# Performance work log

Hardware: AMD Instinct MI355X
Metric: run time of the kernel (lower is better)

Reference implementation:

```python
import jax, jax.numpy as jnp
import numpy as np

B, T, H = 8, 2048, 2048
N = 100000
PROJ = 512
TOP_K = 10
LN_EPS = 1e-5


def setup_inputs() -> dict:
    key = jax.random.key(0)
    ks = jax.random.split(key, 16)
    s = 0.02
    return {
        "x": jax.random.normal(ks[0], (B, T, H), jnp.float32),
        "keys": jax.random.normal(ks[1], (N, H), jnp.float32),
        "confidences": jax.random.uniform(ks[2], (N,), jnp.float32),
        "Wq": jax.random.normal(ks[3], (PROJ, H), jnp.float32) * s,
        "bq": jnp.zeros((PROJ,), jnp.float32),
        "Wk": jax.random.normal(ks[4], (PROJ, H), jnp.float32) * s,
        "bk": jnp.zeros((PROJ,), jnp.float32),
        "Wg": jax.random.normal(ks[5], (H, 2 * H), jnp.float32) * s,
        "bg": jnp.zeros((H,), jnp.float32),
        "Wm1": jax.random.normal(ks[6], (H, 2 * H), jnp.float32) * s,
        "bm1": jnp.zeros((H,), jnp.float32),
        "Wm2": jax.random.normal(ks[7], (H, H), jnp.float32) * s,
        "bm2": jnp.zeros((H,), jnp.float32),
        "gamma": jnp.ones((H,), jnp.float32),
        "beta": jnp.zeros((H,), jnp.float32),
    }


def reference(x, keys, confidences, Wq, bq, Wk, bk, Wg, bg, Wm1, bm1, Wm2, bm2, gamma, beta):
    # query = mean over time: (B, H)
    query = x.mean(axis=1)
    # projections
    q = query @ Wq.T + bq                  # (B, 512)
    k_proj = keys @ Wk.T + bk              # (N, 512)
    # confidence-scaled scores and top-k retrieval
    scores = (q @ k_proj.T) * confidences[None, :]   # (B, N)
    _, top_idx = jax.lax.top_k(scores, TOP_K)        # (B, k)
    retrieved = keys[top_idx]                        # (B, k, H) gather
    mem_summary = retrieved.mean(axis=1)             # (B, H)
    gate_input = jnp.concatenate([query, mem_summary], axis=-1)  # (B, 2H)
    gate = jax.nn.sigmoid(gate_input @ Wg.T + bg)[:, None, :]    # (B, 1, H)
    h = jax.nn.gelu(gate_input @ Wm1.T + bm1, approximate=False)
    mem_integrated = (h @ Wm2.T + bm2)[:, None, :]               # (B, 1, H)
    y = x + gate * mem_integrated
    # LayerNorm over last dim
    mu = y.mean(axis=-1, keepdims=True)
    var = jnp.mean(jnp.square(y - mu), axis=-1, keepdims=True)
    return (y - mu) * jax.lax.rsqrt(var + LN_EPS) * gamma + beta
```

## Files before the change

### kernel.cpp

```cpp
#include <hip/hip_runtime.h>
#include <math.h>

constexpr int B    = 8;
constexpr int T    = 2048;
constexpr int H    = 2048;
constexpr int NK   = 100000;
constexpr int PROJ = 512;
constexpr int TOPK = 10;
constexpr int TCHUNK = 64;
constexpr int TSUB   = T / TCHUNK;
constexpr int NCHUNK = 64;
constexpr int CS     = 1600;

#define NEG_INF -3.4e38f

typedef float vfloat4 __attribute__((ext_vector_type(4)));

__global__ void __launch_bounds__(256) k_partial_sum(const float* __restrict__ x,
                                                     float* __restrict__ partial) {
    int hblk = blockIdx.x & 1;
    int tc   = (blockIdx.x >> 1) & 63;
    int b    = blockIdx.x >> 7;
    int h    = hblk * 1024 + threadIdx.x * 4;
    const float* xp = x + ((size_t)b * T + (size_t)tc * TSUB) * H + h;
    float4 acc = make_float4(0.f, 0.f, 0.f, 0.f);
#pragma unroll 4
    for (int t = 0; t < TSUB; ++t) {
        float4 v = *(const float4*)(xp + (size_t)t * H);
        acc.x += v.x; acc.y += v.y; acc.z += v.z; acc.w += v.w;
    }
    *(float4*)(partial + ((size_t)(b * TCHUNK + tc)) * H + h) = acc;
}

__global__ void __launch_bounds__(256) k_finish_mean(const float* __restrict__ partial,
                                                     float* __restrict__ query,
                                                     float* __restrict__ gi) {
    int idx = blockIdx.x * 256 + threadIdx.x;
    int b = idx >> 11, h = idx & 2047;
    float s = 0.f;
    for (int tc = 0; tc < TCHUNK; ++tc)
        s += partial[((size_t)(b * TCHUNK + tc)) * H + h];
    float m = s * (1.0f / T);
    query[idx] = m;
    gi[(size_t)b * 2 * H + h] = m;
}

__global__ void __launch_bounds__(256) k_q(const float* __restrict__ query,
                                           const float* __restrict__ Wq,
                                           const float* __restrict__ bq,
                                           float* __restrict__ qv) {
    int wave = threadIdx.x >> 6, lane = threadIdx.x & 63;
    int gidx = blockIdx.x * 4 + wave;
    int b = gidx >> 9, p = gidx & 511;
    const float* qr = query + (size_t)b * H;
    const float* wr = Wq + (size_t)p * H;
    float acc = 0.f;
#pragma unroll
    for (int j = lane * 4; j < H; j += 256) {
        float4 a = *(const float4*)(qr + j);
        float4 w = *(const float4*)(wr + j);
        acc += a.x * w.x + a.y * w.y + a.z * w.z + a.w * w.w;
    }
    for (int o = 32; o > 0; o >>= 1) acc += __shfl_down(acc, o, 64);
    if (lane == 0) qv[gidx] = acc + bq[p];
}

__global__ void k_qb(const float* __restrict__ qv, const float* __restrict__ bk,
                     float* __restrict__ qb) {
    int lane = threadIdx.x;
    for (int b = 0; b < B; ++b) {
        float acc = 0.f;
        for (int j = lane; j < PROJ; j += 64) acc += qv[b * PROJ + j] * bk[j];
        for (int o = 32; o > 0; o >>= 1) acc += __shfl_down(acc, o, 64);
        if (lane == 0) qb[b] = acc;
    }
}

__global__ void __launch_bounds__(256) k_qk_partial(const float* __restrict__ qv,
                                                    const float* __restrict__ Wk,
                                                    float* __restrict__ pqk) {
    int hblk = blockIdx.x & 7, pc = blockIdx.x >> 3;
    int h = hblk * 256 + threadIdx.x;
    float acc[B];
#pragma unroll
    for (int b = 0; b < B; ++b) acc[b] = 0.f;
    for (int p = pc * 32; p < pc * 32 + 32; ++p) {
        float w = Wk[(size_t)p * H + h];
#pragma unroll
        for (int b = 0; b < B; ++b) acc[b] += qv[b * PROJ + p] * w;
    }
#pragma unroll
    for (int b = 0; b < B; ++b)
        pqk[((size_t)(pc * B + b)) * H + h] = acc[b];
}

__global__ void __launch_bounds__(256) k_qk_finish(const float* __restrict__ pqk,
                                                   float* __restrict__ qk) {
    int idx = blockIdx.x * 256 + threadIdx.x;
    int b = idx >> 11, h = idx & 2047;
    float s = 0.f;
#pragma unroll
    for (int pc = 0; pc < 16; ++pc) s += pqk[((size_t)(pc * B + b)) * H + h];
    qk[idx] = s;
}

__global__ void __launch_bounds__(512) k_scores(const float* __restrict__ keys,
                                                const float* __restrict__ conf,
                                                const float* __restrict__ qk,
                                                const float* __restrict__ qb,
                                                float* __restrict__ scores) {
    __shared__ float sqk[B * H];
    for (int i = threadIdx.x * 4; i < B * H; i += 2048)
        *(float4*)(sqk + i) = *(const float4*)(qk + i);
    __syncthreads();

    const int wave = threadIdx.x >> 6, lane = threadIdx.x & 63;
    const long r0 = (long)blockIdx.x * 32 + wave * 4;

    float acc[4][B];
#pragma unroll
    for (int r = 0; r < 4; ++r)
#pragma unroll
        for (int b = 0; b < B; ++b) acc[r][b] = 0.f;

#pragma unroll 2
    for (int it = 0; it < 8; ++it) {
        int j = it * 256 + lane * 4;
        vfloat4 kv[4];
#pragma unroll
        for (int r = 0; r < 4; ++r)
            kv[r] = __builtin_nontemporal_load(
                (const vfloat4*)(keys + (size_t)(r0 + r) * H + j));
#pragma unroll
        for (int b = 0; b < B; ++b) {
            float4 w = *(const float4*)(sqk + b * H + j);
#pragma unroll
            for (int r = 0; r < 4; ++r)
                acc[r][b] += kv[r].x * w.x + kv[r].y * w.y + kv[r].z * w.z + kv[r].w * w.w;
        }
    }

#pragma unroll
    for (int r = 0; r < 4; ++r) {
        long n = r0 + r;
#pragma unroll
        for (int b = 0; b < B; ++b) {
            float v = acc[r][b];
            for (int o = 32; o > 0; o >>= 1) v += __shfl_down(v, o, 64);
            if (lane == 0)
                scores[(size_t)b * NK + n] = conf[n] * (v + qb[b]);
        }
    }
}

__global__ void __launch_bounds__(256) k_topk1(const float* __restrict__ scores,
                                               float* __restrict__ candv,
                                               int* __restrict__ candi) {
    const int c = blockIdx.x & (NCHUNK - 1), b = blockIdx.x >> 6;
    const int tid = threadIdx.x, lane = tid & 63, wave = tid >> 6;
    __shared__ float wv[4 * TOPK];
    __shared__ int   wi[4 * TOPK];

    float lv[TOPK];
    int   li[TOPK];
#pragma unroll
    for (int i = 0; i < TOPK; ++i) { lv[i] = NEG_INF; li[i] = 0; }

    const int start = c * CS;
    const int end = (start + CS < NK) ? start + CS : NK;
    for (int n = start + tid; n < end; n += 256) {
        float v = scores[(size_t)b * NK + n];
        if (v > lv[TOPK - 1]) {
            bool m[TOPK];
#pragma unroll
            for (int i = 0; i < TOPK; ++i) m[i] = (lv[i] < v);
#pragma unroll
            for (int i = TOPK - 1; i > 0; --i)
                if (m[i - 1]) { lv[i] = lv[i - 1]; li[i] = li[i - 1]; }
#pragma unroll
            for (int i = 0; i < TOPK; ++i)
                if (m[i] && (i == 0 || !m[i - 1])) { lv[i] = v; li[i] = n; }
        }
    }

    int ptr = 0;
    for (int round = 0; round < TOPK; ++round) {
        float bv = (ptr < TOPK) ? lv[ptr] : NEG_INF;
        int   bi = (ptr < TOPK) ? li[ptr] : 0;
        int   bl = lane;
        for (int o = 32; o > 0; o >>= 1) {
            float ov = __shfl_down(bv, o, 64);
            int   oi = __shfl_down(bi, o, 64);
            int   ol = __shfl_down(bl, o, 64);
            if (ov > bv) { bv = ov; bi = oi; bl = ol; }
        }
        if (lane == 0) { wv[wave * TOPK + round] = bv; wi[wave * TOPK + round] = bi; }
        bl = __shfl(bl, 0, 64);
        if (lane == bl) ptr++;
    }
    __syncthreads();

    if (wave == 0) {
        float v = (lane < 4 * TOPK) ? wv[lane] : NEG_INF;
        int  id = (lane < 4 * TOPK) ? wi[lane] : 0;
        for (int round = 0; round < TOPK; ++round) {
            float bv = v; int bi = id; int bl = lane;
            for (int o = 32; o > 0; o >>= 1) {
                float ov = __shfl_down(bv, o, 64);
                int   oi = __shfl_down(bi, o, 64);
                int   ol = __shfl_down(bl, o, 64);
                if (ov > bv) { bv = ov; bi = oi; bl = ol; }
            }
            if (lane == 0) {
                candv[(size_t)(b * NCHUNK + c) * TOPK + round] = bv;
                candi[(size_t)(b * NCHUNK + c) * TOPK + round] = bi;
            }
            bl = __shfl(bl, 0, 64);
            if (lane == bl) v = NEG_INF;
        }
    }
}

__global__ void __launch_bounds__(64) k_topk2(const float* __restrict__ candv,
                                              const int* __restrict__ candi,
                                              int* __restrict__ topidx) {
    const int b = blockIdx.x, lane = threadIdx.x;
    float lv[TOPK];
    int   li[TOPK];
#pragma unroll
    for (int i = 0; i < TOPK; ++i) { lv[i] = NEG_INF; li[i] = 0; }

#pragma unroll
    for (int r = 0; r < TOPK; ++r) {
        float v = candv[(size_t)b * NCHUNK * TOPK + lane * TOPK + r];
        int  id = candi[(size_t)b * NCHUNK * TOPK + lane * TOPK + r];
        if (v > lv[TOPK - 1]) {
            bool m[TOPK];
#pragma unroll
            for (int i = 0; i < TOPK; ++i) m[i] = (lv[i] < v);
#pragma unroll
            for (int i = TOPK - 1; i > 0; --i)
                if (m[i - 1]) { lv[i] = lv[i - 1]; li[i] = li[i - 1]; }
#pragma unroll
            for (int i = 0; i < TOPK; ++i)
                if (m[i] && (i == 0 || !m[i - 1])) { lv[i] = v; li[i] = id; }
        }
    }

    int ptr = 0;
    for (int round = 0; round < TOPK; ++round) {
        float bv = (ptr < TOPK) ? lv[ptr] : NEG_INF;
        int   bi = (ptr < TOPK) ? li[ptr] : 0;
        int   bl = lane;
        for (int o = 32; o > 0; o >>= 1) {
            float ov = __shfl_down(bv, o, 64);
            int   oi = __shfl_down(bi, o, 64);
            int   ol = __shfl_down(bl, o, 64);
            if (ov > bv) { bv = ov; bi = oi; bl = ol; }
        }
        if (lane == 0) topidx[b * TOPK + round] = bi;
        bl = __shfl(bl, 0, 64);
        if (lane == bl) ptr++;
    }
}

__global__ void __launch_bounds__(256) k_memsum(const float* __restrict__ keys,
                                                const int* __restrict__ topidx,
                                                float* __restrict__ gi) {
    int idx = blockIdx.x * 256 + threadIdx.x;
    int b = idx >> 11, h = idx & 2047;
    float s = 0.f;
#pragma unroll
    for (int i = 0; i < TOPK; ++i) {
        int n = topidx[b * TOPK + i];
        s += keys[(size_t)n * H + h];
    }
    gi[(size_t)b * 2 * H + H + h] = s * (1.0f / TOPK);
}

__global__ void __launch_bounds__(256) k_mlp1(const float* __restrict__ gi,
                                              const float* __restrict__ Wg,
                                              const float* __restrict__ bg,
                                              const float* __restrict__ Wm1,
                                              const float* __restrict__ bm1,
                                              float* __restrict__ gate,
                                              float* __restrict__ h1) {
    int wave = threadIdx.x >> 6, lane = threadIdx.x & 63;
    int row = blockIdx.x * 4 + wave;
    bool isGate = row < H;
    int i = isGate ? row : row - H;
    const float* W = (isGate ? Wg : Wm1) + (size_t)i * 2 * H;

    float acc[B];
#pragma unroll
    for (int b = 0; b < B; ++b) acc[b] = 0.f;

#pragma unroll
    for (int j = lane * 4; j < 2 * H; j += 256) {
        float4 w = *(const float4*)(W + j);
#pragma unroll
        for (int b = 0; b < B; ++b) {
            float4 g = *(const float4*)(gi + (size_t)b * 2 * H + j);
            acc[b] += w.x * g.x + w.y * g.y + w.z * g.z + w.w * g.w;
        }
    }
#pragma unroll
    for (int b = 0; b < B; ++b) {
        float v = acc[b];
        for (int o = 32; o > 0; o >>= 1) v += __shfl_down(v, o, 64);
        if (lane == 0) {
            if (isGate) {
                v += bg[i];
                gate[b * H + i] = 1.0f / (1.0f + expf(-v));
            } else {
                v += bm1[i];
                h1[b * H + i] = 0.5f * v * (1.0f + erff(v * 0.70710678118654752f));
            }
        }
    }
}

__global__ void __launch_bounds__(256) k_mlp2(const float* __restrict__ h1,
                                              const float* __restrict__ Wm2,
                                              const float* __restrict__ bm2,
                                              const float* __restrict__ gate,
                                              float* __restrict__ gm) {
    int wave = threadIdx.x >> 6, lane = threadIdx.x & 63;
    int o = blockIdx.x * 4 + wave;
    const float* W = Wm2 + (size_t)o * H;
    float acc[B];
#pragma unroll
    for (int b = 0; b < B; ++b) acc[b] = 0.f;
#pragma unroll
    for (int j = lane * 4; j < H; j += 256) {
        float4 w = *(const float4*)(W + j);
#pragma unroll
        for (int b = 0; b < B; ++b) {
            float4 hh = *(const float4*)(h1 + (size_t)b * H + j);
            acc[b] += w.x * hh.x + w.y * hh.y + w.z * hh.z + w.w * hh.w;
        }
    }
#pragma unroll
    for (int b = 0; b < B; ++b) {
        float v = acc[b];
        for (int oo = 32; oo > 0; oo >>= 1) v += __shfl_down(v, oo, 64);
        if (lane == 0) gm[b * H + o] = gate[b * H + o] * (v + bm2[o]);
    }
}

__global__ void __launch_bounds__(256) k_final(const float* __restrict__ x,
                                               const float* __restrict__ gm,
                                               const float* __restrict__ gamma,
                                               const float* __restrict__ beta,
                                               float* __restrict__ out) {
    const int lane = threadIdx.x & 63, wave = threadIdx.x >> 6;
    const size_t row = (size_t)blockIdx.x * 4 + wave;
    const int b = (int)(row >> 11);
    const float* xr  = x + row * H;
    const float* gmr = gm + (size_t)b * H;

    vfloat4 y[8];
    float s = 0.f;
#pragma unroll
    for (int it = 0; it < 8; ++it) {
        int j = it * 256 + lane * 4;
        vfloat4 xv = *(const vfloat4*)(xr + j);
        vfloat4 gv = *(const vfloat4*)(gmr + j);
        y[it] = xv + gv;
        s += y[it].x + y[it].y + y[it].z + y[it].w;
    }
#pragma unroll
    for (int o = 32; o > 0; o >>= 1) s += __shfl_xor(s, o, 64);
    const float mu = s * (1.0f / H);

    float s2 = 0.f;
#pragma unroll
    for (int it = 0; it < 8; ++it) {
        vfloat4 d = y[it] - mu;
        y[it] = d;
        s2 += d.x * d.x + d.y * d.y + d.z * d.z + d.w * d.w;
    }
#pragma unroll
    for (int o = 32; o > 0; o >>= 1) s2 += __shfl_xor(s2, o, 64);
    const float inv = rsqrtf(s2 * (1.0f / H) + 1e-5f);

#pragma unroll
    for (int it = 0; it < 8; ++it) {
        int j = it * 256 + lane * 4;
        vfloat4 g = *(const vfloat4*)(gamma + j);
        vfloat4 bb = *(const vfloat4*)(beta + j);
        vfloat4 o_ = y[it] * inv * g + bb;
        __builtin_nontemporal_store(o_, (vfloat4*)(out + row * H + j));
    }
}

extern "C" void kernel_launch(void* const* d_in, const int* in_sizes, int n_in,
                              void* d_out, int out_size, void* d_ws, size_t ws_size,
                              hipStream_t stream) {
    const float* x     = (const float*)d_in[0];
    const float* keys  = (const float*)d_in[1];
    const float* conf  = (const float*)d_in[2];
    const float* Wq    = (const float*)d_in[3];
    const float* bq    = (const float*)d_in[4];
    const float* Wk    = (const float*)d_in[5];
    const float* bk    = (const float*)d_in[6];
    const float* Wg    = (const float*)d_in[7];
    const float* bg    = (const float*)d_in[8];
    const float* Wm1   = (const float*)d_in[9];
    const float* bm1   = (const float*)d_in[10];
    const float* Wm2   = (const float*)d_in[11];
    const float* bm2   = (const float*)d_in[12];
    const float* gamma = (const float*)d_in[13];
    const float* beta  = (const float*)d_in[14];
    float* out = (float*)d_out;

    float* ws = (float*)d_ws;
    float* partial = ws;        ws += (size_t)B * TCHUNK * H;
    float* query   = ws;        ws += B * H;
    float* gi      = ws;        ws += B * 2 * H;
    float* qv      = ws;        ws += B * PROJ;
    float* qb      = ws;        ws += 64;
    float* pqk     = ws;        ws += 16 * B * H;
    float* qk      = ws;        ws += B * H;
    float* scores  = ws;        ws += (size_t)B * NK;
    float* candv   = ws;        ws += B * NCHUNK * TOPK;
    int*   candi   = (int*)ws;  ws += B * NCHUNK * TOPK;
    int*   topidx  = (int*)ws;  ws += 128;
    float* gate    = ws;        ws += B * H;
    float* h1      = ws;        ws += B * H;
    float* gm      = ws;        ws += B * H;

    k_partial_sum<<<B * TCHUNK * 2, 256, 0, stream>>>(x, partial);
    k_finish_mean<<<B * H / 256, 256, 0, stream>>>(partial, query, gi);
    k_q<<<B * PROJ / 4, 256, 0, stream>>>(query, Wq, bq, qv);
    k_qb<<<1, 64, 0, stream>>>(qv, bk, qb);
    k_qk_partial<<<128, 256, 0, stream>>>(qv, Wk, pqk);
    k_qk_finish<<<B * H / 256, 256, 0, stream>>>(pqk, qk);
    k_scores<<<NK / 32, 512, 0, stream>>>(keys, conf, qk, qb, scores);
    k_topk1<<<B * NCHUNK, 256, 0, stream>>>(scores, candv, candi);
    k_topk2<<<B, 64, 0, stream>>>(candv, candi, topidx);
    k_memsum<<<B * H / 256, 256, 0, stream>>>(keys, topidx, gi);
    k_mlp1<<<2 * H / 4, 256, 0, stream>>>(gi, Wg, bg, Wm1, bm1, gate, h1);
    k_mlp2<<<H / 4, 256, 0, stream>>>(h1, Wm2, bm2, gate, gm);
    k_final<<<B * T / 4, 256, 0, stream>>>(x, gm, gamma, beta, out);
}
```

Measured before the change: 365.4 us.

## Fold the small qb and top-k merge kernels into neighbours; add nontemporal x loads

The one-wave qb kernel becomes an extra block appended to k_qk_partial. The second-stage top-k merge moves into k_memsum, where wave 0 of each block merges the per-chunk sorted candidates into shared memory before gathering keys. This removes two tiny serial launches and the topidx round trip. Reads of x in the partial-sum and final LayerNorm kernels now use nontemporal loads, and the scores loop unroll goes from 2 to 4. The cost is redundant merge work in every memsum block and a possible loss of cache reuse of x between the two passes.

```diff
diff --git a/kernel.cpp b/kernel.cpp
--- a/kernel.cpp
+++ b/kernel.cpp
@@ -23,13 +23,13 @@
     int b    = blockIdx.x >> 7;
     int h    = hblk * 1024 + threadIdx.x * 4;
     const float* xp = x + ((size_t)b * T + (size_t)tc * TSUB) * H + h;
-    float4 acc = make_float4(0.f, 0.f, 0.f, 0.f);
+    vfloat4 acc = {0.f, 0.f, 0.f, 0.f};
 #pragma unroll 4
     for (int t = 0; t < TSUB; ++t) {
-        float4 v = *(const float4*)(xp + (size_t)t * H);
-        acc.x += v.x; acc.y += v.y; acc.z += v.z; acc.w += v.w;
-    }
-    *(float4*)(partial + ((size_t)(b * TCHUNK + tc)) * H + h) = acc;
+        vfloat4 v = __builtin_nontemporal_load((const vfloat4*)(xp + (size_t)t * H));
+        acc += v;
+    }
+    *(vfloat4*)(partial + ((size_t)(b * TCHUNK + tc)) * H + h) = acc;
 }
 
 __global__ void __launch_bounds__(256) k_finish_mean(const float* __restrict__ partial,
@@ -65,20 +65,23 @@
     if (lane == 0) qv[gidx] = acc + bq[p];
 }
 
-__global__ void k_qb(const float* __restrict__ qv, const float* __restrict__ bk,
-                     float* __restrict__ qb) {
-    int lane = threadIdx.x;
-    for (int b = 0; b < B; ++b) {
-        float acc = 0.f;
-        for (int j = lane; j < PROJ; j += 64) acc += qv[b * PROJ + j] * bk[j];
-        for (int o = 32; o > 0; o >>= 1) acc += __shfl_down(acc, o, 64);
-        if (lane == 0) qb[b] = acc;
-    }
-}
-
 __global__ void __launch_bounds__(256) k_qk_partial(const float* __restrict__ qv,
                                                     const float* __restrict__ Wk,
-                                                    float* __restrict__ pqk) {
+                                                    const float* __restrict__ bk,
+                                                    float* __restrict__ pqk,
+                                                    float* __restrict__ qb) {
+    if (blockIdx.x == 128) {
+        int lane = threadIdx.x & 63;
+        if (threadIdx.x < 64) {
+            for (int b = 0; b < B; ++b) {
+                float acc = 0.f;
+                for (int j = lane; j < PROJ; j += 64) acc += qv[b * PROJ + j] * bk[j];
+                for (int o = 32; o > 0; o >>= 1) acc += __shfl_down(acc, o, 64);
+                if (lane == 0) qb[b] = acc;
+            }
+        }
+        return;
+    }
     int hblk = blockIdx.x & 7, pc = blockIdx.x >> 3;
     int h = hblk * 256 + threadIdx.x;
     float acc[B];
@@ -123,7 +126,7 @@
 #pragma unroll
         for (int b = 0; b < B; ++b) acc[r][b] = 0.f;
 
-#pragma unroll 2
+#pragma unroll 4
     for (int it = 0; it < 8; ++it) {
         int j = it * 256 + lane * 4;
         vfloat4 kv[4];
@@ -221,58 +224,46 @@
     }
 }
 
-__global__ void __launch_bounds__(64) k_topk2(const float* __restrict__ candv,
-                                              const int* __restrict__ candi,
-                                              int* __restrict__ topidx) {
-    const int b = blockIdx.x, lane = threadIdx.x;
-    float lv[TOPK];
-    int   li[TOPK];
-#pragma unroll
-    for (int i = 0; i < TOPK; ++i) { lv[i] = NEG_INF; li[i] = 0; }
-
-#pragma unroll
-    for (int r = 0; r < TOPK; ++r) {
-        float v = candv[(size_t)b * NCHUNK * TOPK + lane * TOPK + r];
-        int  id = candi[(size_t)b * NCHUNK * TOPK + lane * TOPK + r];
-        if (v > lv[TOPK - 1]) {
-            bool m[TOPK];
-#pragma unroll
-            for (int i = 0; i < TOPK; ++i) m[i] = (lv[i] < v);
-#pragma unroll
-            for (int i = TOPK - 1; i > 0; --i)
-                if (m[i - 1]) { lv[i] = lv[i - 1]; li[i] = li[i - 1]; }
-#pragma unroll
-            for (int i = 0; i < TOPK; ++i)
-                if (m[i] && (i == 0 || !m[i - 1])) { lv[i] = v; li[i] = id; }
-        }
-    }
-
-    int ptr = 0;
-    for (int round = 0; round < TOPK; ++round) {
-        float bv = (ptr < TOPK) ? lv[ptr] : NEG_INF;
-        int   bi = (ptr < TOPK) ? li[ptr] : 0;
-        int   bl = lane;
-        for (int o = 32; o > 0; o >>= 1) {
-            float ov = __shfl_down(bv, o, 64);
-            int   oi = __shfl_down(bi, o, 64);
-            int   ol = __shfl_down(bl, o, 64);
-            if (ov > bv) { bv = ov; bi = oi; bl = ol; }
-        }
-        if (lane == 0) topidx[b * TOPK + round] = bi;
-        bl = __shfl(bl, 0, 64);
-        if (lane == bl) ptr++;
-    }
-}
-
 __global__ void __launch_bounds__(256) k_memsum(const float* __restrict__ keys,
-                                                const int* __restrict__ topidx,
+                                                const float* __restrict__ candv,
+                                                const int* __restrict__ candi,
                                                 float* __restrict__ gi) {
-    int idx = blockIdx.x * 256 + threadIdx.x;
-    int b = idx >> 11, h = idx & 2047;
+    const int blk = blockIdx.x;
+    const int b = (blk * 256) >> 11;
+    const int tid = threadIdx.x, lane = tid & 63, wave = tid >> 6;
+    __shared__ int stop[TOPK];
+
+    if (wave == 0) {
+        float lv[TOPK];
+        int   li[TOPK];
+#pragma unroll
+        for (int r = 0; r < TOPK; ++r) {
+            lv[r] = candv[(size_t)(b * NCHUNK + lane) * TOPK + r];
+            li[r] = candi[(size_t)(b * NCHUNK + lane) * TOPK + r];
+        }
+        int ptr = 0;
+        for (int round = 0; round < TOPK; ++round) {
+            float bv = (ptr < TOPK) ? lv[ptr] : NEG_INF;
+            int   bi = (ptr < TOPK) ? li[ptr] : 0;
+            int   bl = lane;
+            for (int o = 32; o > 0; o >>= 1) {
+                float ov = __shfl_down(bv, o, 64);
+                int   oi = __shfl_down(bi, o, 64);
+                int   ol = __shfl_down(bl, o, 64);
+                if (ov > bv) { bv = ov; bi = oi; bl = ol; }
+            }
+            if (lane == 0) stop[round] = bi;
+            bl = __shfl(bl, 0, 64);
+            if (lane == bl) ptr++;
+        }
+    }
+    __syncthreads();
+
+    int h = (blk * 256 + tid) & 2047;
     float s = 0.f;
 #pragma unroll
     for (int i = 0; i < TOPK; ++i) {
-        int n = topidx[b * TOPK + i];
+        int n = stop[i];
         s += keys[(size_t)n * H + h];
     }
     gi[(size_t)b * 2 * H + H + h] = s * (1.0f / TOPK);
@@ -364,7 +355,7 @@
 #pragma unroll
     for (int it = 0; it < 8; ++it) {
         int j = it * 256 + lane * 4;
-        vfloat4 xv = *(const vfloat4*)(xr + j);
+        vfloat4 xv = __builtin_nontemporal_load((const vfloat4*)(xr + j));
         vfloat4 gv = *(const vfloat4*)(gmr + j);
         y[it] = xv + gv;
         s += y[it].x + y[it].y + y[it].z + y[it].w;
@@ -425,7 +416,6 @@
     float* scores  = ws;        ws += (size_t)B * NK;
     float* candv   = ws;        ws += B * NCHUNK * TOPK;
     int*   candi   = (int*)ws;  ws += B * NCHUNK * TOPK;
-    int*   topidx  = (int*)ws;  ws += 128;
     float* gate    = ws;        ws += B * H;
     float* h1      = ws;        ws += B * H;
     float* gm      = ws;        ws += B * H;
@@ -433,13 +423,11 @@
     k_partial_sum<<<B * TCHUNK * 2, 256, 0, stream>>>(x, partial);
     k_finish_mean<<<B * H / 256, 256, 0, stream>>>(partial, query, gi);
     k_q<<<B * PROJ / 4, 256, 0, stream>>>(query, Wq, bq, qv);
-    k_qb<<<1, 64, 0, stream>>>(qv, bk, qb);
-    k_qk_partial<<<128, 256, 0, stream>>>(qv, Wk, pqk);
+    k_qk_partial<<<129, 256, 0, stream>>>(qv, Wk, bk, pqk, qb);
     k_qk_finish<<<B * H / 256, 256, 0, stream>>>(pqk, qk);
     k_scores<<<NK / 32, 512, 0, stream>>>(keys, conf, qk, qb, scores);
     k_topk1<<<B * NCHUNK, 256, 0, stream>>>(scores, candv, candi);
-    k_topk2<<<B, 64, 0, stream>>>(candv, candi, topidx);
-    k_memsum<<<B * H / 256, 256, 0, stream>>>(keys, topidx, gi);
+    k_memsum<<<B * H / 256, 256, 0, stream>>>(keys, candv, candi, gi);
     k_mlp1<<<2 * H / 4, 256, 0, stream>>>(gi, Wg, bg, Wm1, bm1, gate, h1);
     k_mlp2<<<H / 4, 256, 0, stream>>>(h1, Wm2, bm2, gate, gm);
     k_final<<<B * T / 4, 256, 0, stream>>>(x, gm, gamma, beta, out);
```

After: 365.7 us. About the same (+0.1%).
